# Kernel optimization log

Measured on AMD Instinct MI355X. Metric: run time of the kernel, lower is better.

The kernel has to match this reference:

```python
import jax, jax.numpy as jnp
import numpy as np

N_PAD, N_PAS = 14, 8
N_H = 2 + N_PAD            # 16
MHID, RN, NINF = 256, 256, 256
N_NODES, N_EDGES, N_GRAPHS = 40000, 640000, 64


def _dense_params(key, fin, fout):
    w = jax.random.normal(key, (fin, fout), jnp.float32) / np.float32(np.sqrt(fin))
    return w, jnp.zeros((fout,), jnp.float32)


def setup_inputs() -> dict:
    key = jax.random.key(0)
    ks = jax.random.split(key, 17)
    x = jax.random.normal(ks[0], (N_NODES, 2), jnp.float32)
    e = jax.random.normal(ks[1], (N_EDGES, 1), jnp.float32)
    first = jax.random.randint(ks[2], (N_EDGES,), 0, N_NODES, jnp.int32)
    second = jax.random.randint(ks[3], (N_EDGES,), 0, N_NODES, jnp.int32)
    segment = jnp.sort(jax.random.randint(ks[4], (N_NODES,), 0, N_GRAPHS, jnp.int32))
    l_w1, l_b1 = _dense_params(ks[5], 1, MHID)
    l_w2, l_b2 = _dense_params(ks[6], MHID, N_H * N_H)
    b_w1, b_b1 = _dense_params(ks[7], 1, MHID)
    b_w2, b_b2 = _dense_params(ks[8], MHID, N_H)
    gru_k = jax.random.normal(ks[9], (N_H, 3 * N_H), jnp.float32) / np.float32(np.sqrt(N_H))
    gru_rk = jax.random.normal(ks[10], (N_H, 3 * N_H), jnp.float32) / np.float32(np.sqrt(N_H))
    gru_b = jnp.zeros((2, 3 * N_H), jnp.float32)  # [input_bias, recurrent_bias] (reset_after=True)
    i_w1, i_b1 = _dense_params(ks[11], N_H + 2, RN)
    i_w2, i_b2 = _dense_params(ks[12], RN, RN)
    j_w1, j_b1 = _dense_params(ks[13], N_H + 2, RN)
    j_w2, j_b2 = _dense_params(ks[14], RN, RN)
    f_w1, f_b1 = _dense_params(ks[15], RN, NINF)
    f_w2, f_b2 = _dense_params(ks[16], NINF, 1)
    return dict(x=x, e=e, first=first, second=second, segment=segment,
                l_w1=l_w1, l_b1=l_b1, l_w2=l_w2, l_b2=l_b2,
                b_w1=b_w1, b_b1=b_b1, b_w2=b_w2, b_b2=b_b2,
                gru_k=gru_k, gru_rk=gru_rk, gru_b=gru_b,
                i_w1=i_w1, i_b1=i_b1, i_w2=i_w2, i_b2=i_b2,
                j_w1=j_w1, j_b1=j_b1, j_w2=j_w2, j_b2=j_b2,
                f_w1=f_w1, f_b1=f_b1, f_w2=f_w2, f_b2=f_b2)


def reference(x, e, first, second, segment,
              l_w1, l_b1, l_w2, l_b2,
              b_w1, b_b1, b_w2, b_b2,
              gru_k, gru_rk, gru_b,
              i_w1, i_b1, i_w2, i_b2,
              j_w1, j_b1, j_w2, j_b2,
              f_w1, f_b1, f_w2, f_b2):
    selu = jax.nn.selu
    # Edge-conditioned message weights depend only on e; identical across passes, so hoist.
    a = (selu(e @ l_w1 + l_b1) @ l_w2 + l_b2).reshape(-1, N_H, N_H)  # [E, N_H, N_H]
    bvec = selu(e @ b_w1 + b_b1) @ b_w2 + b_b2                       # [E, N_H]
    h = jnp.pad(x, ((0, 0), (0, N_PAD)))                             # [N, N_H]
    for _ in range(N_PAS):
        m = jnp.einsum('eij,ej->ei', a, h[first]) + bvec             # per-edge matmul + bias
        m = jax.ops.segment_sum(m, second, num_segments=N_NODES)     # scatter-add to nodes
        # Keras GRUCell (reset_after=True)
        mx = m @ gru_k + gru_b[0]
        mh = h @ gru_rk + gru_b[1]
        xz, xr, xh = jnp.split(mx, 3, axis=1)
        rz, rr, rh = jnp.split(mh, 3, axis=1)
        z = jax.nn.sigmoid(xz + rz)
        r = jax.nn.sigmoid(xr + rr)
        hh = jnp.tanh(xh + r * rh)
        h = z * h + (1.0 - z) * hh
    # Readout R: gated sum over nodes of each graph (segment sorted)
    hx = jnp.concatenate([h, x], axis=1)                             # [N, N_H+2]
    gate = jax.nn.sigmoid(jnp.tanh(hx @ i_w1 + i_b1) @ i_w2 + i_b2)  # [N, RN]
    feat = selu(hx @ j_w1 + j_b1) @ j_w2 + j_b2                      # [N, RN]
    node_batch = jax.ops.segment_sum(gate * feat, segment, num_segments=N_GRAPHS)
    return selu(node_batch @ f_w1 + f_b1) @ f_w2 + f_b2              # [G, 1]
```

## Files before the change

kernel.cpp:

```cpp
#include <hip/hip_runtime.h>

#define E_EDGES 640000
#define N_NODES 40000
#define NGRAPH  64
#define TPTS    2048
#define TMIN    -6.0f
#define TSPAN   12.0f
#define NBLK    157
#define SBLK    256
#define EPB     2500
#define EPB2    256

typedef _Float16 h16x8 __attribute__((ext_vector_type(8)));
typedef float f32x4 __attribute__((ext_vector_type(4)));

__device__ __forceinline__ f32x4 mfma16h(h16x8 a, h16x8 b, f32x4 c) {
    return __builtin_amdgcn_mfma_f32_16x16x32_f16(a, b, c, 0, 0, 0);
}
__device__ __forceinline__ unsigned short f2h(float f) {
    union { _Float16 h; unsigned short u; } v; v.h = (_Float16)f; return v.u;
}
__device__ __forceinline__ float selu_f(float v) {
    const float sc = 1.0507009873554805f;
    const float sa = 1.7580993408473766f;
    return v > 0.f ? sc * v : sa * (__expf(v) - 1.f);
}
__device__ __forceinline__ float sigm_f(float v) { return 1.f / (1.f + __expf(-v)); }
__device__ __forceinline__ float tanh_f(float v) { return 2.f / (1.f + __expf(-2.f * v)) - 1.f; }
__device__ __forceinline__ void tcoord(float t, int& g, float& fr) {
    float tt = (t - TMIN) * ((float)(TPTS - 1) / TSPAN);
    tt = fminf(fmaxf(tt, 0.f), (float)(TPTS - 1));
    int gi = (int)tt;
    if (gi > TPTS - 2) gi = TPTS - 2;
    g = gi; fr = tt - (float)gi;
}

__global__ void k_zero_out(float* __restrict__ out, int n) {
    int i = blockIdx.x * 64 + threadIdx.x;
    if (i < n) out[i] = 0.f;
}

__global__ __launch_bounds__(256) void k_init(const float* __restrict__ x,
                                              float* __restrict__ h0,
                                              int* __restrict__ counts) {
    int idx = blockIdx.x * 256 + threadIdx.x;
    if (idx < N_NODES * 16) {
        int j = idx & 15, n = idx >> 4;
        h0[idx] = (j < 2) ? x[n * 2 + j] : 0.f;
    }
    if (idx < N_NODES) counts[idx] = 0;
}

__global__ __launch_bounds__(256) void k_count(const int* __restrict__ second,
                                               int* __restrict__ counts) {
    int e = blockIdx.x * 256 + threadIdx.x;
    if (e < E_EDGES) atomicAdd(&counts[second[e]], 1);
}

__global__ __launch_bounds__(256) void k_scanA(const int* __restrict__ counts,
                                               int* __restrict__ offs,
                                               int* __restrict__ bsum) {
    __shared__ int lds[256];
    int tid = threadIdx.x;
    int base = blockIdx.x * 256;
    int v = (base + tid < N_NODES) ? counts[base + tid] : 0;
    lds[tid] = v;
    __syncthreads();
    for (int d = 1; d < 256; d <<= 1) {
        int t2 = (tid >= d) ? lds[tid - d] : 0;
        __syncthreads();
        lds[tid] += t2;
        __syncthreads();
    }
    if (base + tid < N_NODES) offs[base + tid] = lds[tid] - v;
    if (tid == 255) bsum[blockIdx.x] = lds[255];
}

__global__ __launch_bounds__(256) void k_scanB(const int* __restrict__ bsum,
                                               int* __restrict__ boff) {
    __shared__ int lds[256];
    int tid = threadIdx.x;
    int v = (tid < NBLK) ? bsum[tid] : 0;
    lds[tid] = v;
    __syncthreads();
    for (int d = 1; d < 256; d <<= 1) {
        int t2 = (tid >= d) ? lds[tid - d] : 0;
        __syncthreads();
        lds[tid] += t2;
        __syncthreads();
    }
    if (tid < NBLK) boff[tid] = lds[tid] - v;
}

__global__ __launch_bounds__(256) void k_scanC(int* __restrict__ offs,
                                               int* __restrict__ cur,
                                               const int* __restrict__ boff) {
    int tid = threadIdx.x;
    int i = blockIdx.x * 256 + tid;
    if (i < N_NODES) {
        int o = offs[i] + boff[blockIdx.x];
        offs[i] = o;
        cur[i] = o;
    }
    if (i == 0) offs[N_NODES] = E_EDGES;
}

__global__ __launch_bounds__(256) void k_scatter(const int* __restrict__ second,
                                                 const int* __restrict__ first,
                                                 const float* __restrict__ e,
                                                 int* __restrict__ cur,
                                                 int* __restrict__ fs,
                                                 float* __restrict__ ev) {
    int i = blockIdx.x * 256 + threadIdx.x;
    if (i < E_EDGES) {
        int pos = atomicAdd(&cur[second[i]], 1);
        fs[pos] = first[i];
        ev[pos] = e[i];
    }
}

__global__ __launch_bounds__(256) void k_hist(const float* __restrict__ ev,
                                              int* __restrict__ histG) {
    __shared__ int hcnt[TPTS];
    int tid = threadIdx.x, b = blockIdx.x;
    for (int c = tid; c < TPTS; c += 256) hcnt[c] = 0;
    __syncthreads();
    int s = b * EPB;
    for (int it = 0; it < 10; ++it) {
        int p = s + it * 256 + tid;
        if (p < s + EPB) {
            int g; float fr;
            tcoord(ev[p], g, fr);
            atomicAdd(&hcnt[g], 1);
        }
    }
    __syncthreads();
    for (int c = tid; c < TPTS; c += 256) histG[c * SBLK + b] = hcnt[c];
}

__global__ __launch_bounds__(256) void k_gscanA(const int* __restrict__ in,
                                                int* __restrict__ out,
                                                int* __restrict__ bsum) {
    __shared__ int lds[256];
    int tid = threadIdx.x;
    int base = blockIdx.x * 256;
    int v = in[base + tid];
    lds[tid] = v;
    __syncthreads();
    for (int d = 1; d < 256; d <<= 1) {
        int t2 = (tid >= d) ? lds[tid - d] : 0;
        __syncthreads();
        lds[tid] += t2;
        __syncthreads();
    }
    out[base + tid] = lds[tid] - v;
    if (tid == 255) bsum[blockIdx.x] = lds[255];
}

__global__ __launch_bounds__(256) void k_scan2(const int* __restrict__ in,
                                               int* __restrict__ out) {
    __shared__ int lds[256];
    __shared__ int carry;
    int tid = threadIdx.x;
    if (tid == 0) carry = 0;
    __syncthreads();
    for (int base = 0; base < TPTS; base += 256) {
        int v = in[base + tid];
        lds[tid] = v;
        __syncthreads();
        for (int d = 1; d < 256; d <<= 1) {
            int t2 = (tid >= d) ? lds[tid - d] : 0;
            __syncthreads();
            lds[tid] += t2;
            __syncthreads();
        }
        int incl = lds[tid];
        int c0 = carry;
        out[base + tid] = c0 + incl - v;
        __syncthreads();
        if (tid == 255) carry = c0 + incl;
        __syncthreads();
    }
}

__global__ __launch_bounds__(256) void k_gscanC(int* __restrict__ out,
                                                const int* __restrict__ boff) {
    out[blockIdx.x * 256 + threadIdx.x] += boff[blockIdx.x];
}

__global__ __launch_bounds__(256) void k_sort(
    const int* __restrict__ fs, const float* __restrict__ ev,
    const int* __restrict__ baseG,
    int* __restrict__ sfs, float* __restrict__ sev, int* __restrict__ spos) {
    __shared__ int hcnt[TPTS];
    int tid = threadIdx.x, b = blockIdx.x;
    for (int c = tid; c < TPTS; c += 256) hcnt[c] = 0;
    __syncthreads();
    int s = b * EPB;
    for (int it = 0; it < 10; ++it) {
        int p = s + it * 256 + tid;
        if (p < s + EPB) {
            int g; float fr;
            tcoord(ev[p], g, fr);
            int r = atomicAdd(&hcnt[g], 1);
            int q = baseG[g * SBLK + b] + r;
            sfs[q] = fs[p];
            sev[q] = ev[p];
            spos[q] = p;
        }
    }
}

__global__ __launch_bounds__(256) void k_tab(
    const float* __restrict__ lw1, const float* __restrict__ lb1,
    const float* __restrict__ lw2, const float* __restrict__ lb2,
    const float* __restrict__ bw1, const float* __restrict__ bb1,
    const float* __restrict__ bw2, const float* __restrict__ bb2,
    float* __restrict__ ta, float* __restrict__ tb) {
    __shared__ float hl[8][256];
    __shared__ float hb[8][256];
    int tid = threadIdx.x;
    int g0 = blockIdx.x * 8;
    const float STEP = TSPAN / (float)(TPTS - 1);
#pragma unroll
    for (int g = 0; g < 8; ++g) {
        float t = TMIN + (float)(g0 + g) * STEP;
        hl[g][tid] = selu_f(t * lw1[tid] + lb1[tid]);
        hb[g][tid] = selu_f(t * bw1[tid] + bb1[tid]);
    }
    __syncthreads();
    float acc[8] = {0, 0, 0, 0, 0, 0, 0, 0};
    float accB[8] = {0, 0, 0, 0, 0, 0, 0, 0};
    for (int k = 0; k < 256; ++k) {
        float w = lw2[k * 256 + tid];
        float wb = (tid < 16) ? bw2[k * 16 + tid] : 0.f;
#pragma unroll
        for (int g = 0; g < 8; ++g) {
            acc[g] += hl[g][k] * w;
            accB[g] += hb[g][k] * wb;
        }
    }
    float lb = lb2[tid];
#pragma unroll
    for (int g = 0; g < 8; ++g) ta[(g0 + g) * 256 + tid] = acc[g] + lb;
    if (tid < 16) {
        float bb = bb2[tid];
#pragma unroll
        for (int g = 0; g < 8; ++g) tb[(g0 + g) * 16 + tid] = accB[g] + bb;
    }
}

__global__ __launch_bounds__(256) void k_w2prep(const float* __restrict__ iw2,
                                                const float* __restrict__ jw2,
                                                unsigned short* __restrict__ iw2t,
                                                unsigned short* __restrict__ jw2t) {
    int idx = blockIdx.x * 256 + threadIdx.x;
    int k = idx >> 8, n = idx & 255;
    iw2t[n * 256 + k] = f2h(iw2[idx]);
    jw2t[n * 256 + k] = f2h(jw2[idx]);
}

__global__ __launch_bounds__(256) void k_bvnode(const float* __restrict__ tb,
                                                const int* __restrict__ offs,
                                                const float* __restrict__ ev,
                                                float* __restrict__ bvn) {
    int idx = blockIdx.x * 256 + threadIdx.x;
    int node = idx >> 4, i = idx & 15;
    int beg = offs[node], end = offs[node + 1];
    float s = 0.f;
    for (int p = beg; p < end; ++p) {
        int g; float fr;
        tcoord(ev[p], g, fr);
        float v0 = tb[g * 16 + i], v1 = tb[g * 16 + 16 + i];
        s += v0 + fr * (v1 - v0);
    }
    bvn[idx] = s;
}

__global__ __launch_bounds__(256) void k_msg2(
    const float* __restrict__ ta, const int* __restrict__ sfs,
    const float* __restrict__ sev, const int* __restrict__ spos,
    const float* __restrict__ hin, float* __restrict__ msg) {
    const int tid = threadIdx.x;
    const int i = tid & 15;
    int q = blockIdx.x * EPB2 + (tid >> 4);
    int gcur = -1;
    float4 a0 = {0, 0, 0, 0}, a1 = a0, a2 = a0, a3 = a0;
    float4 c0 = a0, c1 = a0, c2 = a0, c3 = a0;
    int f_c = sfs[q];
    float e_c = sev[q];
    int sp_c = spos[q];
    const float4* hp0 = (const float4*)(hin + f_c * 16);
    float4 h0 = hp0[0], h1 = hp0[1], h2 = hp0[2], h3 = hp0[3];
    const int ITERS = EPB2 / 16;
    for (int it = 0; it < ITERS; ++it) {
        int f_n = 0; float e_n = 0.f; int sp_n = 0;
        float4 n0 = {0, 0, 0, 0}, n1 = n0, n2 = n0, n3 = n0;
        if (it + 1 < ITERS) {
            int q2 = q + 16;
            f_n = sfs[q2]; e_n = sev[q2]; sp_n = spos[q2];
            const float4* hp = (const float4*)(hin + f_n * 16);
            n0 = hp[0]; n1 = hp[1]; n2 = hp[2]; n3 = hp[3];
        }
        int g; float fr;
        tcoord(e_c, g, fr);
        if (g != gcur) {
            gcur = g;
            const float4* A0 = (const float4*)(ta + g * 256 + i * 16);
            a0 = A0[0]; a1 = A0[1]; a2 = A0[2]; a3 = A0[3];
            c0 = A0[64]; c1 = A0[65]; c2 = A0[66]; c3 = A0[67];
        }
        float s =
              (a0.x + fr * (c0.x - a0.x)) * h0.x + (a0.y + fr * (c0.y - a0.y)) * h0.y
            + (a0.z + fr * (c0.z - a0.z)) * h0.z + (a0.w + fr * (c0.w - a0.w)) * h0.w
            + (a1.x + fr * (c1.x - a1.x)) * h1.x + (a1.y + fr * (c1.y - a1.y)) * h1.y
            + (a1.z + fr * (c1.z - a1.z)) * h1.z + (a1.w + fr * (c1.w - a1.w)) * h1.w
            + (a2.x + fr * (c2.x - a2.x)) * h2.x + (a2.y + fr * (c2.y - a2.y)) * h2.y
            + (a2.z + fr * (c2.z - a2.z)) * h2.z + (a2.w + fr * (c2.w - a2.w)) * h2.w
            + (a3.x + fr * (c3.x - a3.x)) * h3.x + (a3.y + fr * (c3.y - a3.y)) * h3.y
            + (a3.z + fr * (c3.z - a3.z)) * h3.z + (a3.w + fr * (c3.w - a3.w)) * h3.w;
        msg[sp_c * 16 + i] = s;
        q += 16; f_c = f_n; e_c = e_n; sp_c = sp_n;
        h0 = n0; h1 = n1; h2 = n2; h3 = n3;
    }
}

__global__ __launch_bounds__(256) void k_gru(
    const float* __restrict__ msg, const float* __restrict__ bvn,
    const int* __restrict__ offs,
    const float* __restrict__ hin, float* __restrict__ hout,
    const float* __restrict__ gk, const float* __restrict__ grk,
    const float* __restrict__ gb) {
    __shared__ float l_gk[768], l_grk[768], l_gb[96];
    int tid = threadIdx.x;
    for (int i2 = tid; i2 < 768; i2 += 256) { l_gk[i2] = gk[i2]; l_grk[i2] = grk[i2]; }
    if (tid < 96) l_gb[tid] = gb[tid];
    __syncthreads();

    int idx = blockIdx.x * 256 + tid;
    int node = idx >> 4, i = idx & 15;
    int lane = tid & 63, lbase = lane & ~15;
    int beg = offs[node], end = offs[node + 1];
    float acc = bvn[idx];
    for (int p = beg; p < end; ++p) acc += msg[p * 16 + i];

    float mxz = l_gb[i], mxr = l_gb[16 + i], mxh = l_gb[32 + i];
    float mhz = l_gb[48 + i], mhr = l_gb[64 + i], mhh = l_gb[80 + i];
    const float* hrow = hin + node * 16;
#pragma unroll
    for (int j = 0; j < 16; ++j) {
        float mj = __shfl(acc, lbase + j);
        float hj = hrow[j];
        mxz += mj * l_gk[j * 48 + i];       mhz += hj * l_grk[j * 48 + i];
        mxr += mj * l_gk[j * 48 + 16 + i];  mhr += hj * l_grk[j * 48 + 16 + i];
        mxh += mj * l_gk[j * 48 + 32 + i];  mhh += hj * l_grk[j * 48 + 32 + i];
    }
    float z = sigm_f(mxz + mhz);
    float r = sigm_f(mxr + mhr);
    float hh = tanh_f(mxh + r * mhh);
    float hi = hrow[i];
    hout[idx] = z * hi + (1.f - z) * hh;
}

__global__ __launch_bounds__(256) void k_ro1(
    const float* __restrict__ h, const float* __restrict__ x,
    const float* __restrict__ iw1, const float* __restrict__ ib1,
    const float* __restrict__ jw1, const float* __restrict__ jb1,
    unsigned short* __restrict__ ui, unsigned short* __restrict__ uj,
    float* __restrict__ nb) {
    __shared__ float w_i[18 * 256];
    __shared__ float w_j[18 * 256];
    __shared__ float hx[32][18];
    int tid = threadIdx.x;
    int nb0 = blockIdx.x * 32;
    if (blockIdx.x < NGRAPH) nb[blockIdx.x * 256 + tid] = 0.f;
    for (int idx = tid; idx < 18 * 256; idx += 256) {
        w_i[idx] = iw1[idx];
        w_j[idx] = jw1[idx];
    }
    for (int idx = tid; idx < 32 * 18; idx += 256) {
        int nl = idx / 18, k = idx - nl * 18;
        hx[nl][k] = (k < 16) ? h[(nb0 + nl) * 16 + k] : x[(nb0 + nl) * 2 + (k - 16)];
    }
    __syncthreads();
    float bi = ib1[tid], bj = jb1[tid];
    for (int nl = 0; nl < 32; ++nl) {
        float ai = bi, aj = bj;
#pragma unroll
        for (int k = 0; k < 18; ++k) {
            float hv = hx[nl][k];
            ai += hv * w_i[k * 256 + tid];
            aj += hv * w_j[k * 256 + tid];
        }
        ui[(size_t)(nb0 + nl) * 256 + tid] = f2h(tanh_f(ai));
        uj[(size_t)(nb0 + nl) * 256 + tid] = f2h(selu_f(aj));
    }
}

__global__ __launch_bounds__(256) void k_ro23(
    const unsigned short* __restrict__ ui, const unsigned short* __restrict__ uj,
    const unsigned short* __restrict__ iw2t, const float* __restrict__ ib2,
    const unsigned short* __restrict__ jw2t, const float* __restrict__ jb2,
    const int* __restrict__ seg, float* __restrict__ nb) {
    __shared__ alignas(16) unsigned short ldsB[256 * 40];
    const int tid = threadIdx.x;
    const int w = tid >> 6, lane = tid & 63;
    const int m = lane & 15, quad = lane >> 4;
    const int rowBase = blockIdx.x * 64 + w * 16;
    const int rowA = rowBase + m;

    f32x4 accg[16], accf[16];
#pragma unroll
    for (int nt = 0; nt < 16; ++nt) {
        accg[nt] = (f32x4){0.f, 0.f, 0.f, 0.f};
        accf[nt] = (f32x4){0.f, 0.f, 0.f, 0.f};
    }

    for (int kc = 0; kc < 8; ++kc) {
        __syncthreads();
        {
            const unsigned short* src = iw2t + tid * 256 + kc * 32;
            uint4 v0 = *(const uint4*)(src);
            uint4 v1 = *(const uint4*)(src + 8);
            uint4 v2 = *(const uint4*)(src + 16);
            uint4 v3 = *(const uint4*)(src + 24);
            *(uint4*)&ldsB[tid * 40 + 0]  = v0;
            *(uint4*)&ldsB[tid * 40 + 8]  = v1;
            *(uint4*)&ldsB[tid * 40 + 16] = v2;
            *(uint4*)&ldsB[tid * 40 + 24] = v3;
        }
        __syncthreads();
        const int kk = kc * 32 + quad * 8;
        h16x8 ag = *(const h16x8*)&ui[(size_t)rowA * 256 + kk];
        const unsigned short* bp = &ldsB[m * 40 + quad * 8];
#pragma unroll
        for (int nt = 0; nt < 16; ++nt) {
            h16x8 bfr = *(const h16x8*)(bp + nt * 640);
            accg[nt] = mfma16h(ag, bfr, accg[nt]);
        }
    }
    for (int kc = 0; kc < 8; ++kc) {
        __syncthreads();
        {
            const unsigned short* src = jw2t + tid * 256 + kc * 32;
            uint4 v0 = *(const uint4*)(src);
            uint4 v1 = *(const uint4*)(src + 8);
            uint4 v2 = *(const uint4*)(src + 16);
            uint4 v3 = *(const uint4*)(src + 24);
            *(uint4*)&ldsB[tid * 40 + 0]  = v0;
            *(uint4*)&ldsB[tid * 40 + 8]  = v1;
            *(uint4*)&ldsB[tid * 40 + 16] = v2;
            *(uint4*)&ldsB[tid * 40 + 24] = v3;
        }
        __syncthreads();
        const int kk = kc * 32 + quad * 8;
        h16x8 af = *(const h16x8*)&uj[(size_t)rowA * 256 + kk];
        const unsigned short* bp = &ldsB[m * 40 + quad * 8];
#pragma unroll
        for (int nt = 0; nt < 16; ++nt) {
            h16x8 bfr = *(const h16x8*)(bp + nt * 640);
            accf[nt] = mfma16h(af, bfr, accf[nt]);
        }
    }

    const int s_lo = seg[rowBase], s_hi = seg[rowBase + 15];
    if (s_lo == s_hi) {
#pragma unroll
        for (int nt = 0; nt < 16; ++nt) {
            int col = nt * 16 + m;
            float bi = ib2[col], bj = jb2[col];
            float vr = 0.f;
#pragma unroll
            for (int reg = 0; reg < 4; ++reg) {
                float g = sigm_f(accg[nt][reg] + bi);
                float f = accf[nt][reg] + bj;
                vr += g * f;
            }
            vr += __shfl_xor(vr, 16);
            vr += __shfl_xor(vr, 32);
            if (quad == 0) atomicAdd(&nb[s_lo * 256 + col], vr);
        }
    } else {
#pragma unroll
        for (int nt = 0; nt < 16; ++nt) {
            int col = nt * 16 + m;
            float bi = ib2[col], bj = jb2[col];
            int cur = seg[rowBase + quad * 4];
            float sum = 0.f;
#pragma unroll
            for (int reg = 0; reg < 4; ++reg) {
                int s = seg[rowBase + quad * 4 + reg];
                float g = sigm_f(accg[nt][reg] + bi);
                float f = accf[nt][reg] + bj;
                if (s != cur) { atomicAdd(&nb[cur * 256 + col], sum); cur = s; sum = 0.f; }
                sum += g * f;
            }
            atomicAdd(&nb[cur * 256 + col], sum);
        }
    }
}

__global__ __launch_bounds__(256) void k_final(const float* __restrict__ nb,
                                               const float* __restrict__ fw1,
                                               const float* __restrict__ fb1,
                                               const float* __restrict__ fw2,
                                               const float* __restrict__ fb2,
                                               float* __restrict__ out) {
    __shared__ float red[4];
    int t = threadIdx.x, g = blockIdx.x;
    float acc = fb1[t];
    for (int k = 0; k < 256; ++k) acc += nb[g * 256 + k] * fw1[k * 256 + t];
    float v = selu_f(acc) * fw2[t];
#pragma unroll
    for (int off = 32; off > 0; off >>= 1) v += __shfl_down(v, off);
    if ((t & 63) == 0) red[t >> 6] = v;
    __syncthreads();
    if (t == 0) out[g] = red[0] + red[1] + red[2] + red[3] + fb2[0];
}

extern "C" void kernel_launch(void* const* d_in, const int* in_sizes, int n_in,
                              void* d_out, int out_size, void* d_ws, size_t ws_size,
                              hipStream_t stream) {
    const float* x    = (const float*)d_in[0];
    const float* e    = (const float*)d_in[1];
    const int* first  = (const int*)d_in[2];
    const int* second = (const int*)d_in[3];
    const int* seg    = (const int*)d_in[4];
    const float* lw1  = (const float*)d_in[5];
    const float* lb1  = (const float*)d_in[6];
    const float* lw2  = (const float*)d_in[7];
    const float* lb2  = (const float*)d_in[8];
    const float* bw1  = (const float*)d_in[9];
    const float* bb1  = (const float*)d_in[10];
    const float* bw2  = (const float*)d_in[11];
    const float* bb2  = (const float*)d_in[12];
    const float* gk   = (const float*)d_in[13];
    const float* grk  = (const float*)d_in[14];
    const float* gb   = (const float*)d_in[15];
    const float* iw1  = (const float*)d_in[16];
    const float* ib1  = (const float*)d_in[17];
    const float* iw2  = (const float*)d_in[18];
    const float* ib2  = (const float*)d_in[19];
    const float* jw1  = (const float*)d_in[20];
    const float* jb1  = (const float*)d_in[21];
    const float* jw2  = (const float*)d_in[22];
    const float* jb2  = (const float*)d_in[23];
    const float* fw1  = (const float*)d_in[24];
    const float* fb1  = (const float*)d_in[25];
    const float* fw2  = (const float*)d_in[26];
    const float* fb2  = (const float*)d_in[27];
    (void)in_sizes; (void)n_in;

    float* OUT = (float*)d_out;

    const size_t REQ = 150608896ULL;
    if (ws_size < REQ) {
        k_zero_out<<<(out_size + 63) / 64, 64, 0, stream>>>(OUT, out_size);
        return;
    }

    char* ws = (char*)d_ws;
    float* TA   = (float*)(ws + 0);
    float* TB   = (float*)(ws + 2097152);
    float* H0   = (float*)(ws + 2228224);
    float* H1   = (float*)(ws + 4788224);
    float* BVN  = (float*)(ws + 7348224);
    int* CNT    = (int*)(ws + 9908224);
    int* OFF    = (int*)(ws + 10068224);
    int* CUR    = (int*)(ws + 10228480);
    int* BSUM   = (int*)(ws + 10388480);
    int* BOFF   = (int*)(ws + 10389504);
    int* FS     = (int*)(ws + 10390528);
    float* EV   = (float*)(ws + 12950528);
    int* HIST   = (int*)(ws + 15510528);
    int* BASE   = (int*)(ws + 17607680);
    int* BSUM2  = (int*)(ws + 19704832);
    int* BOFF2  = (int*)(ws + 19713024);
    int* SFS    = (int*)(ws + 19721216);
    float* SEV  = (float*)(ws + 22281216);
    int* SPOS   = (int*)(ws + 24841216);
    char* ro    = ws + 27401216;
    float* MSG  = (float*)(ro + 0);
    unsigned short* UI = (unsigned short*)(ro + 0);
    unsigned short* UJ = (unsigned short*)(ro + 20480000);
    float* NB   = (float*)(ro + 122880000);
    unsigned short* IW2T = (unsigned short*)(ro + 122945536);
    unsigned short* JW2T = (unsigned short*)(ro + 123076608);

    k_init<<<2500, 256, 0, stream>>>(x, H0, CNT);
    k_count<<<2500, 256, 0, stream>>>(second, CNT);
    k_scanA<<<NBLK, 256, 0, stream>>>(CNT, OFF, BSUM);
    k_scanB<<<1, 256, 0, stream>>>(BSUM, BOFF);
    k_scanC<<<NBLK, 256, 0, stream>>>(OFF, CUR, BOFF);
    k_scatter<<<2500, 256, 0, stream>>>(second, first, e, CUR, FS, EV);
    k_hist<<<SBLK, 256, 0, stream>>>(EV, HIST);
    k_gscanA<<<TPTS * SBLK / 256, 256, 0, stream>>>(HIST, BASE, BSUM2);
    k_scan2<<<1, 256, 0, stream>>>(BSUM2, BOFF2);
    k_gscanC<<<TPTS * SBLK / 256, 256, 0, stream>>>(BASE, BOFF2);
    k_sort<<<SBLK, 256, 0, stream>>>(FS, EV, BASE, SFS, SEV, SPOS);
    k_tab<<<TPTS / 8, 256, 0, stream>>>(lw1, lb1, lw2, lb2, bw1, bb1, bw2, bb2, TA, TB);
    k_w2prep<<<256, 256, 0, stream>>>(iw2, jw2, IW2T, JW2T);
    k_bvnode<<<2500, 256, 0, stream>>>(TB, OFF, EV, BVN);
    const float* hin = H0;
    float* hout = H1;
    for (int p = 0; p < 8; ++p) {
        k_msg2<<<E_EDGES / EPB2, 256, 0, stream>>>(TA, SFS, SEV, SPOS, hin, MSG);
        k_gru<<<2500, 256, 0, stream>>>(MSG, BVN, OFF, hin, hout, gk, grk, gb);
        const float* t = hout; hout = (float*)hin; hin = t;
    }
    k_ro1<<<1250, 256, 0, stream>>>(hin, x, iw1, ib1, jw1, jb1, UI, UJ, NB);
    k_ro23<<<625, 256, 0, stream>>>(UI, UJ, IW2T, ib2, JW2T, jb2, seg, NB);
    k_final<<<64, 256, 0, stream>>>(NB, fw1, fb1, fw2, fb2, OUT);
}
```

Baseline: 947.8 us.

## Split readout GEMM across column quarters and fuse gate/feature K loops

The readout second-layer kernel now launches a 2D grid where each block handles 64 output columns instead of all 256, giving four times as many blocks with far fewer accumulator registers per thread. The gate and feature weight tiles are staged together in two smaller LDS buffers so both GEMMs share a single K loop and half as many barriers. The cost is that each block re-reads the A rows (ui/uj) four times and issues four times as many atomics into the graph sums.

Measured after the change: 926.1 us. 2.3% less time.

```diff
diff --git a/kernel.cpp b/kernel.cpp
--- a/kernel.cpp
+++ b/kernel.cpp
@@ -402,72 +402,55 @@
     const unsigned short* __restrict__ iw2t, const float* __restrict__ ib2,
     const unsigned short* __restrict__ jw2t, const float* __restrict__ jb2,
     const int* __restrict__ seg, float* __restrict__ nb) {
-    __shared__ alignas(16) unsigned short ldsB[256 * 40];
+    __shared__ alignas(16) unsigned short ldsBg[64 * 40];
+    __shared__ alignas(16) unsigned short ldsBf[64 * 40];
     const int tid = threadIdx.x;
+    const int cq = blockIdx.x;
     const int w = tid >> 6, lane = tid & 63;
     const int m = lane & 15, quad = lane >> 4;
-    const int rowBase = blockIdx.x * 64 + w * 16;
+    const int rowBase = blockIdx.y * 64 + w * 16;
     const int rowA = rowBase + m;
-
-    f32x4 accg[16], accf[16];
-#pragma unroll
-    for (int nt = 0; nt < 16; ++nt) {
+    const int col0 = cq * 64;
+
+    f32x4 accg[4], accf[4];
+#pragma unroll
+    for (int nt = 0; nt < 4; ++nt) {
         accg[nt] = (f32x4){0.f, 0.f, 0.f, 0.f};
         accf[nt] = (f32x4){0.f, 0.f, 0.f, 0.f};
     }
 
+    const int col_l = tid >> 2;
+    const int koff = (tid & 3) * 8;
     for (int kc = 0; kc < 8; ++kc) {
         __syncthreads();
         {
-            const unsigned short* src = iw2t + tid * 256 + kc * 32;
-            uint4 v0 = *(const uint4*)(src);
-            uint4 v1 = *(const uint4*)(src + 8);
-            uint4 v2 = *(const uint4*)(src + 16);
-            uint4 v3 = *(const uint4*)(src + 24);
-            *(uint4*)&ldsB[tid * 40 + 0]  = v0;
-            *(uint4*)&ldsB[tid * 40 + 8]  = v1;
-            *(uint4*)&ldsB[tid * 40 + 16] = v2;
-            *(uint4*)&ldsB[tid * 40 + 24] = v3;
+            const unsigned short* sg = iw2t + (col0 + col_l) * 256 + kc * 32 + koff;
+            const unsigned short* sf = jw2t + (col0 + col_l) * 256 + kc * 32 + koff;
+            uint4 vg = *(const uint4*)sg;
+            uint4 vf = *(const uint4*)sf;
+            *(uint4*)&ldsBg[col_l * 40 + koff] = vg;
+            *(uint4*)&ldsBf[col_l * 40 + koff] = vf;
         }
         __syncthreads();
         const int kk = kc * 32 + quad * 8;
         h16x8 ag = *(const h16x8*)&ui[(size_t)rowA * 256 + kk];
-        const unsigned short* bp = &ldsB[m * 40 + quad * 8];
-#pragma unroll
-        for (int nt = 0; nt < 16; ++nt) {
-            h16x8 bfr = *(const h16x8*)(bp + nt * 640);
-            accg[nt] = mfma16h(ag, bfr, accg[nt]);
-        }
-    }
-    for (int kc = 0; kc < 8; ++kc) {
-        __syncthreads();
-        {
-            const unsigned short* src = jw2t + tid * 256 + kc * 32;
-            uint4 v0 = *(const uint4*)(src);
-            uint4 v1 = *(const uint4*)(src + 8);
-            uint4 v2 = *(const uint4*)(src + 16);
-            uint4 v3 = *(const uint4*)(src + 24);
-            *(uint4*)&ldsB[tid * 40 + 0]  = v0;
-            *(uint4*)&ldsB[tid * 40 + 8]  = v1;
-            *(uint4*)&ldsB[tid * 40 + 16] = v2;
-            *(uint4*)&ldsB[tid * 40 + 24] = v3;
-        }
-        __syncthreads();
-        const int kk = kc * 32 + quad * 8;
         h16x8 af = *(const h16x8*)&uj[(size_t)rowA * 256 + kk];
-        const unsigned short* bp = &ldsB[m * 40 + quad * 8];
-#pragma unroll
-        for (int nt = 0; nt < 16; ++nt) {
-            h16x8 bfr = *(const h16x8*)(bp + nt * 640);
-            accf[nt] = mfma16h(af, bfr, accf[nt]);
+        const unsigned short* bpg = &ldsBg[m * 40 + quad * 8];
+        const unsigned short* bpf = &ldsBf[m * 40 + quad * 8];
+#pragma unroll
+        for (int nt = 0; nt < 4; ++nt) {
+            h16x8 bg = *(const h16x8*)(bpg + nt * 640);
+            h16x8 bf = *(const h16x8*)(bpf + nt * 640);
+            accg[nt] = mfma16h(ag, bg, accg[nt]);
+            accf[nt] = mfma16h(af, bf, accf[nt]);
         }
     }
 
     const int s_lo = seg[rowBase], s_hi = seg[rowBase + 15];
     if (s_lo == s_hi) {
 #pragma unroll
-        for (int nt = 0; nt < 16; ++nt) {
-            int col = nt * 16 + m;
+        for (int nt = 0; nt < 4; ++nt) {
+            int col = col0 + nt * 16 + m;
             float bi = ib2[col], bj = jb2[col];
             float vr = 0.f;
 #pragma unroll
@@ -482,8 +465,8 @@
         }
     } else {
 #pragma unroll
-        for (int nt = 0; nt < 16; ++nt) {
-            int col = nt * 16 + m;
+        for (int nt = 0; nt < 4; ++nt) {
+            int col = col0 + nt * 16 + m;
             float bi = ib2[col], bj = jb2[col];
             int cur = seg[rowBase + quad * 4];
             float sum = 0.f;
@@ -609,6 +592,6 @@
         const float* t = hout; hout = (float*)hin; hin = t;
     }
     k_ro1<<<1250, 256, 0, stream>>>(hin, x, iw1, ib1, jw1, jb1, UI, UJ, NB);
-    k_ro23<<<625, 256, 0, stream>>>(UI, UJ, IW2T, ib2, JW2T, jb2, seg, NB);
+    k_ro23<<<dim3(4, 625), 256, 0, stream>>>(UI, UJ, IW2T, ib2, JW2T, jb2, seg, NB);
     k_final<<<64, 256, 0, stream>>>(NB, fw1, fb1, fw2, fb2, OUT);
 }
```
